# Kernel tuning notes

Measured on AMD Instinct MI355X. Metric: run time of the kernel, lower is better.

Reference implementation:

```python
import jax, jax.numpy as jnp
import numpy as np

B, N, D = 64, 197, 768
H, HD = 12, 64
MAX_REL = 14
SCALE = HD ** -0.5


def rel_indices(n, max_rel):
    """Static 2D relative-position index matrices of shape (n, n), int32."""
    lq = n - 1
    side = int(lq ** 0.5)
    r = np.arange(lq)
    dv = r[None, :] // side - r[:, None] // side
    dh = r[None, :] % side - r[:, None] % side
    fv = np.clip(dv, -max_rel, max_rel) + max_rel + 1
    fh = np.clip(dh, -max_rel, max_rel) + max_rel + 1
    # pad one row/col of zeros on top-left for the cls token (index 0)
    fv = np.pad(fv, ((1, 0), (1, 0)), constant_values=0)
    fh = np.pad(fh, ((1, 0), (1, 0)), constant_values=0)
    return fv.astype(np.int32), fh.astype(np.int32)


IDX_V, IDX_H = rel_indices(N, MAX_REL)


def setup_inputs() -> dict:
    key = jax.random.key(0)
    ks = jax.random.split(key, 13)
    lin = lambda k: jax.random.normal(k, (D, H * HD), jnp.float32) * 0.02
    tab = lambda k: jax.random.normal(k, (2 * MAX_REL + 2, HD), jnp.float32) * 0.02
    return {
        'x': jax.random.normal(ks[0], (B, N, D), jnp.float32),
        'wq': lin(ks[1]), 'bq': jnp.zeros((H * HD,), jnp.float32),
        'wk': lin(ks[2]), 'bk': jnp.zeros((H * HD,), jnp.float32),
        'wv': lin(ks[3]), 'bv': jnp.zeros((H * HD,), jnp.float32),
        'wp': jax.random.normal(ks[4], (H * HD, D), jnp.float32) * 0.02,
        'bp': jnp.zeros((D,), jnp.float32),
        'rel_k_v': tab(ks[5]), 'rel_k_h': tab(ks[6]),
        'rel_v_v': tab(ks[7]), 'rel_v_h': tab(ks[8]),
    }


def reference(x, wq, bq, wk, bk, wv, bv, wp, bp, rel_k_v, rel_k_h, rel_v_v, rel_v_h):
    b, n, _ = x.shape
    # qkv projections -> (B, H, N, HD)
    q = (x @ wq + bq).reshape(b, n, H, HD).transpose(0, 2, 1, 3)
    k = (x @ wk + bk).reshape(b, n, H, HD).transpose(0, 2, 1, 3)
    v = (x @ wv + bv).reshape(b, n, H, HD).transpose(0, 2, 1, 3)

    attn = jnp.einsum('bhid,bhjd->bhij', q, k) * SCALE
    # iRPE key bias: gather (N, N, HD) table then contract with q per query pos
    r_p_k = rel_k_v[IDX_V] + rel_k_h[IDX_H]              # (N, N, HD)
    attn = attn + jnp.einsum('bhid,ijd->bhij', q, r_p_k) * SCALE
    attn = jax.nn.softmax(attn, axis=-1)

    out = jnp.einsum('bhij,bhjd->bhid', attn, v)
    # iRPE value bias
    r_p_v = rel_v_v[IDX_V] + rel_v_h[IDX_H]              # (N, N, HD)
    out = out + jnp.einsum('bhij,ijd->bhid', attn, r_p_v)

    out = out.transpose(0, 2, 1, 3).reshape(b, n, H * HD)
    return out @ wp + bp
```

## Files before the change

kernel.cpp:

```cpp
#include <hip/hip_runtime.h>
#include <math.h>

#define SCALE_ 0.125f

typedef unsigned short u16;
typedef __attribute__((ext_vector_type(8))) _Float16 half8;
typedef __attribute__((ext_vector_type(4))) float f32x4;
#define MFMA_H __builtin_amdgcn_mfma_f32_16x16x32_f16

__device__ __forceinline__ u16 f2h(float f) {
    union { _Float16 h; u16 u; } v; v.h = (_Float16)f; return v.u;
}
__device__ __forceinline__ float h2f(u16 u) {
    union { _Float16 h; u16 u; } v; v.u = u; return (float)v.h;
}
__device__ __forceinline__ void gload16(const u16* g, u16* l) {
    __builtin_amdgcn_global_load_lds(
        (const __attribute__((address_space(1))) void*)g,
        (__attribute__((address_space(3))) void*)l, 16, 0, 0);
}
__device__ __forceinline__ half8 ld_h8(const u16* p) {
    return *(const half8*)p;
}

__global__ void prep_all(const float* __restrict__ x,
                         const float* __restrict__ w0, const float* __restrict__ w1,
                         const float* __restrict__ w2, const float* __restrict__ w3,
                         const float* __restrict__ rkv, const float* __restrict__ rkh,
                         const float* __restrict__ rvv, const float* __restrict__ rvh,
                         u16* __restrict__ xh,
                         u16* o0, u16* o1, u16* o2, u16* o3,
                         u16* __restrict__ tk, u16* __restrict__ gt,
                         u16* __restrict__ khot, u16* __restrict__ vtp) {
    __shared__ float t[64 * 68];
    int b = blockIdx.x;
    const int tid = threadIdx.x;

    if (b < 4728) {
        size_t idx = ((size_t)b * 256 + tid) * 8;
        float4 a = *(const float4*)(x + idx), bb = *(const float4*)(x + idx + 4);
        float f[8] = {a.x, a.y, a.z, a.w, bb.x, bb.y, bb.z, bb.w};
        u16 hs[8];
        #pragma unroll
        for (int e = 0; e < 8; ++e) hs[e] = f2h(f[e]);
        *(uint4*)(xh + idx) = *(uint4*)hs;
        return;
    }
    b -= 4728;
    if (b < 576) {
        int z = b / 144, rem = b - z * 144;
        int by = rem / 12, bx = rem - by * 12;
        const float* W; u16* oh;
        if (z == 0)      { W = w0; oh = o0; }
        else if (z == 1) { W = w1; oh = o1; }
        else if (z == 2) { W = w2; oh = o2; }
        else             { W = w3; oh = o3; }
        int k0 = by * 64, n0 = bx * 64;
        #pragma unroll
        for (int rr = 0; rr < 4; ++rr) {
            int r = (tid >> 4) + rr * 16;
            int c = (tid & 15) * 4;
            *(float4*)&t[r * 68 + c] = *(const float4*)(W + (size_t)(k0 + r) * 768 + n0 + c);
        }
        __syncthreads();
        int n = tid >> 2, kc = (tid & 3) * 16;
        u16 hs[16];
        #pragma unroll
        for (int e = 0; e < 16; ++e) hs[e] = f2h(t[(kc + e) * 68 + n]);
        size_t o = (size_t)(n0 + n) * 768 + k0 + kc;
        *(uint4*)(oh + o) = *(uint4*)hs;
        *(uint4*)(oh + o + 8) = *(uint4*)(hs + 8);
        return;
    }
    b -= 576;
    if (b < 16) {
        int idx = b * 256 + tid;
        int r = idx >> 6, d = idx & 63;
        float tv = 0.f;
        if (r < 30) tv = rkv[r * 64 + d];
        else if (r >= 32 && r < 62) tv = rkh[(r - 32) * 64 + d];
        tk[idx] = f2h(tv);
        return;
    }
    b -= 16;
    if (b < 28) {
        int idx = b * 256 + tid;
        int g = idx / 224, j = idx - (idx / 224) * 224;
        float v = 0.f;
        if (j >= 1 && j < 197) {
            int jq = j - 1;
            int jv = jq / 14, jh = jq - jv * 14;
            if (g < 14) v = (jv == g) ? 1.f : 0.f;
            else if (g >= 16 && g < 30) v = (jh == g - 16) ? 1.f : 0.f;
        }
        gt[idx] = f2h(v);
        return;
    }
    b -= 28;
    if (b < 28) {
        int idx = b * 256 + tid;
        int j = idx >> 5, c = idx & 31;
        float v = 0.f;
        if (j >= 1 && j < 197) {
            int jq = j - 1;
            int jv = jq / 14, jh = jq - jv * 14;
            if (c < 14) v = (jv == c) ? 1.f : 0.f;
            else if (c < 28) v = (jh == c - 14) ? 1.f : 0.f;
        }
        khot[idx] = f2h(v);
        return;
    }
    b -= 28;
    {
        u16* vb = vtp + (size_t)b * 64 * 288;
        for (int tt = tid; tt < 64 * 91; tt += 256) {
            int d = tt / 91;
            int c = 197 + (tt - d * 91);
            u16 val = 0;
            if (c >= 208 && c < 272) {
                int rr = c - 208;
                float v = 0.f;
                if (rr < 30) v = rvv[rr * 64 + d];
                else if (rr >= 32 && rr < 62) v = rvh[(rr - 32) * 64 + d];
                val = f2h(v);
            }
            vb[d * 288 + c] = val;
        }
    }
}

__global__ __launch_bounds__(256) void vtrans(const u16* __restrict__ v,
                                              u16* __restrict__ vt) {
    __shared__ u16 L[64 * 72];
    const int bh = blockIdx.x;
    const u16* src = v + (size_t)bh * 197 * 64;
    u16* dst = vt + (size_t)bh * 64 * 288;
    const int tid = threadIdx.x;
    const int keyl = tid >> 2;
    const int c8 = (tid & 3) * 16;
    for (int k0 = 0; k0 < 197; k0 += 64) {
        __syncthreads();
        int key = k0 + keyl;
        if (key < 197) {
            uint4 g0 = *(const uint4*)(src + key * 64 + c8);
            uint4 g1 = *(const uint4*)(src + key * 64 + c8 + 8);
            u16 t0[8]; *(uint4*)t0 = g0;
            u16 t1[8]; *(uint4*)t1 = g1;
            #pragma unroll
            for (int e = 0; e < 8; ++e) L[(c8 + e) * 72 + keyl] = t0[e];
            #pragma unroll
            for (int e = 0; e < 8; ++e) L[(c8 + 8 + e) * 72 + keyl] = t1[e];
        }
        __syncthreads();
        int d = tid >> 2, cc = (tid & 3) * 16;
        if (k0 + cc < 197) {
            int nvalid = min(16, 197 - k0 - cc);
            if (nvalid == 16) {
                *(uint4*)(dst + d * 288 + k0 + cc)     = *(const uint4*)&L[d * 72 + cc];
                *(uint4*)(dst + d * 288 + k0 + cc + 8) = *(const uint4*)&L[d * 72 + cc + 8];
            } else {
                for (int e = 0; e < nvalid; ++e)
                    dst[d * 288 + k0 + cc + e] = L[d * 72 + cc + e];
            }
        }
    }
}

__global__ __launch_bounds__(256, 4) void gemm_f16(
    const u16* __restrict__ Ah,
    const u16* __restrict__ B0, const u16* __restrict__ B1, const u16* __restrict__ B2,
    const float* __restrict__ bias0, const float* __restrict__ bias1,
    const float* __restrict__ bias2,
    u16* qo, u16* ko, u16* vo, float* outf, int nz, int kind)
{
    __shared__ u16 SM[128 * 64 * 2];
    u16* As = SM;
    u16* Bs = SM + 128 * 64;

    const int p = blockIdx.x;
    const int xcd = p & 7, s = p >> 3;
    const int mcnt = (xcd < 3) ? 13 : 12;
    const int mbase = (xcd < 3) ? xcd * 13 : 39 + (xcd - 3) * 12;
    const int jn = 6 * nz;
    if (s >= mcnt * jn) return;
    const int mb = mbase + s / jn;
    const int j = s % jn;
    const int z = j / 6;
    const int nb = j % 6;

    const u16* Bt = B0; const float* bias = bias0;
    if (z == 1) { Bt = B1; bias = bias1; }
    else if (z == 2) { Bt = B2; bias = bias2; }

    const int m0 = mb * 128, n0 = nb * 128;
    const int tid = threadIdx.x;
    const int w = tid >> 6, lane = tid & 63, quad = lane >> 4, l16 = lane & 15;
    const int wm = (w >> 1) * 64, wn = (w & 1) * 64;
    const int rl8 = lane >> 3, cs = lane & 7;
    const int csrc = (cs ^ rl8) * 8;

    f32x4 acc[4][4];
    #pragma unroll
    for (int a = 0; a < 4; ++a)
        #pragma unroll
        for (int b = 0; b < 4; ++b) acc[a][b] = (f32x4){0, 0, 0, 0};

    for (int kt = 0; kt < 768; kt += 64) {
        __syncthreads();
        #pragma unroll
        for (int i = 0; i < 4; ++i) {
            int r = w * 32 + i * 8 + rl8;
            int arow = min(m0 + r, 12607);
            gload16(Ah + (size_t)arow * 768 + kt + csrc, &As[(w * 32 + i * 8) * 64]);
            gload16(Bt + (size_t)(n0 + r) * 768 + kt + csrc, &Bs[(w * 32 + i * 8) * 64]);
        }
        __syncthreads();
        #pragma unroll
        for (int kb = 0; kb < 2; ++kb) {
            const int slot = ((kb * 4 + quad) ^ (l16 & 7)) * 8;
            half8 ah[4], bf[4];
            #pragma unroll
            for (int mi = 0; mi < 4; ++mi) {
                ah[mi] = ld_h8(&As[(wm + mi * 16 + l16) * 64 + slot]);
                bf[mi] = ld_h8(&Bs[(wn + mi * 16 + l16) * 64 + slot]);
            }
            #pragma unroll
            for (int ni = 0; ni < 4; ++ni)
                #pragma unroll
                for (int mi = 0; mi < 4; ++mi)
                    acc[mi][ni] = MFMA_H(ah[mi], bf[ni], acc[mi][ni], 0, 0, 0);
        }
    }

    if (kind == 1) {
        #pragma unroll
        for (int mi = 0; mi < 4; ++mi) {
            #pragma unroll
            for (int r = 0; r < 4; ++r) {
                int gr = m0 + wm + mi * 16 + quad * 4 + r;
                if (gr >= 12608) continue;
                #pragma unroll
                for (int ni = 0; ni < 4; ++ni) {
                    int gc = n0 + wn + ni * 16 + l16;
                    outf[(size_t)gr * 768 + gc] = acc[mi][ni][r] + bias[gc];
                }
            }
        }
        return;
    }

    __syncthreads();
    u16* Cs = SM;
    #pragma unroll
    for (int mi = 0; mi < 4; ++mi) {
        #pragma unroll
        for (int ni = 0; ni < 4; ++ni) {
            int col = wn + ni * 16 + l16;
            float bv = bias[n0 + col];
            #pragma unroll
            for (int r = 0; r < 4; ++r)
                Cs[(wm + mi * 16 + quad * 4 + r) * 128 + col] = f2h(acc[mi][ni][r] + bv);
        }
    }
    __syncthreads();
    u16* O = (z == 0) ? qo : ((z == 1) ? ko : vo);
    int row = tid >> 1, halfc = tid & 1;
    int gr = m0 + row;
    if (gr < 12608) {
        int bb = gr / 197, ii = gr - bb * 197;
        int h = (n0 >> 6) + halfc;
        u16* dst = O + ((size_t)(bb * 12 + h) * 197 + ii) * 64;
        const u16* src = &Cs[row * 128 + halfc * 64];
        #pragma unroll
        for (int e = 0; e < 8; ++e)
            *(uint4*)(dst + e * 8) = *(const uint4*)(src + e * 8);
    }
}

__global__ __launch_bounds__(512, 3) void attn_mfma(
    const u16* __restrict__ qh, const u16* __restrict__ kh,
    const u16* __restrict__ tk, const u16* __restrict__ vt,
    const u16* __restrict__ gt, const u16* __restrict__ khot,
    u16* __restrict__ oh)
{
    __shared__ u16 Ph[64 * 296];
    __shared__ float BsT[64 * 36];
    __shared__ float red[64 * 4];
    u16* Tvh16 = (u16*)BsT;
    u16* Kst = Ph;

    const int p = blockIdx.x;
    const int xcd = p & 7, s = p >> 3;
    const int bh = xcd * 96 + (s >> 2);
    const int qt = s & 3;
    const int I0 = qt * 64;
    const int tid = threadIdx.x;
    const int w = tid >> 6, lane = tid & 63, quad = lane >> 4, l16 = lane & 15;
    const int mf = w >> 1, nh = w & 1;
    const int mr0 = mf * 16;
    const size_t base = (size_t)bh * 197 * 64;
    const uint4 z4 = make_uint4(0, 0, 0, 0);

    half8 qa[2];
    {
        int i = I0 + mr0 + l16;
        bool ok = i < 197;
        const u16* qp = qh + base + (size_t)i * 64 + quad * 8;
        #pragma unroll
        for (int kb = 0; kb < 2; ++kb) {
            uint4 a = ok ? *(const uint4*)(qp + kb * 32) : z4;
            *(uint4*)&qa[kb] = a;
        }
    }
    int jj[7];
    #pragma unroll
    for (int s1 = 0; s1 < 7; ++s1) jj[s1] = (nh * 7 + s1) * 16 + l16;
    half8 kfh[7];
    #pragma unroll
    for (int s1 = 0; s1 < 7; ++s1)
        kfh[s1] = ld_h8(khot + jj[s1] * 32 + quad * 8);
    uint4 kreg[4];
    #pragma unroll
    for (int t2 = 0; t2 < 4; ++t2) {
        int t = tid + t2 * 512;
        int row = t >> 3, chunk = t & 7;
        kreg[t2] = (t < 1792 && row < 197)
                 ? *(const uint4*)(kh + base + (size_t)row * 64 + chunk * 8) : z4;
    }

    #pragma unroll
    for (int s2 = 0; s2 < 2; ++s2) {
        int c = (nh * 2 + s2) * 16 + l16;
        f32x4 acc = (f32x4){0, 0, 0, 0};
        #pragma unroll
        for (int kb = 0; kb < 2; ++kb) {
            half8 th = ld_h8(tk + c * 64 + kb * 32 + quad * 8);
            acc = MFMA_H(qa[kb], th, acc, 0, 0, 0);
        }
        #pragma unroll
        for (int r = 0; r < 4; ++r)
            Tvh16[(mr0 + quad * 4 + r) * 68 + c] = f2h(acc[r]);
    }

    #pragma unroll
    for (int t2 = 0; t2 < 4; ++t2) {
        int t = tid + t2 * 512;
        if (t < 1792) {
            int row = t >> 3, chunk = t & 7;
            *(uint4*)&Kst[row * 72 + chunk * 8] = kreg[t2];
        }
    }
    __syncthreads();

    half8 qa2;
    {
        int m = mr0 + l16;
        int i = I0 + m;
        u16 vals[8];
        if (i >= 1 && i < 197) {
            int qi = i - 1;
            int iv = qi / 14, ih = qi - iv * 14;
            #pragma unroll
            for (int e = 0; e < 8; ++e) {
                int c = quad * 8 + e;
                u16 v = 0;
                if (c < 14)      v = Tvh16[m * 68 + (c - iv + 15)];
                else if (c < 28) v = Tvh16[m * 68 + 32 + ((c - 14) - ih + 15)];
                vals[e] = v;
            }
        } else {
            #pragma unroll
            for (int e = 0; e < 8; ++e) vals[e] = 0;
        }
        *(uint4*)&qa2 = *(uint4*)vals;
    }

    f32x4 sacc[7];
    #pragma unroll
    for (int s1 = 0; s1 < 7; ++s1) {
        int j = jj[s1];
        f32x4 c = MFMA_H(qa[0], ld_h8(&Kst[j * 72 + quad * 8]),
                         (f32x4){0, 0, 0, 0}, 0, 0, 0);
        c = MFMA_H(qa[1], ld_h8(&Kst[j * 72 + 32 + quad * 8]), c, 0, 0, 0);
        c = MFMA_H(qa2, kfh[s1], c, 0, 0, 0);
        sacc[s1] = c;
    }

    #pragma unroll
    for (int r = 0; r < 4; ++r) {
        float mx = sacc[0][r];
        #pragma unroll
        for (int s1 = 1; s1 < 7; ++s1) mx = fmaxf(mx, sacc[s1][r]);
        mx *= SCALE_;
        #pragma unroll
        for (int off = 1; off < 16; off <<= 1) mx = fmaxf(mx, __shfl_xor(mx, off, 64));
        if (l16 == 0) red[(mr0 + quad * 4 + r) * 4 + nh] = mx;
    }
    __syncthreads();

    #pragma unroll
    for (int r = 0; r < 4; ++r) {
        int m = mr0 + quad * 4 + r;
        float M = fmaxf(red[m * 4], red[m * 4 + 1]);
        float sum = 0.f;
        #pragma unroll
        for (int s1 = 0; s1 < 7; ++s1) {
            float pv = (jj[s1] < 197) ? __expf(sacc[s1][r] * SCALE_ - M) : 0.f;
            sacc[s1][r] = pv;
            sum += pv;
        }
        #pragma unroll
        for (int off = 1; off < 16; off <<= 1) sum += __shfl_xor(sum, off, 64);
        if (l16 == 0) red[m * 4 + 2 + nh] = sum;
    }
    #pragma unroll
    for (int s1 = 0; s1 < 7; ++s1) {
        int j = jj[s1];
        if (j < 208) {
            #pragma unroll
            for (int r = 0; r < 4; ++r)
                Ph[(mr0 + quad * 4 + r) * 296 + j] = f2h(sacc[s1][r]);
        }
    }
    #pragma unroll
    for (int t = 0; t < 2; ++t) {
        int ii2 = tid + t * 512;
        Ph[(ii2 >> 4) * 296 + 208 + (ii2 & 15)] = 0;
    }
    __syncthreads();

    {
        f32x4 bacc = (f32x4){0, 0, 0, 0};
        #pragma unroll
        for (int ks = 0; ks < 7; ++ks) {
            half8 ap = ld_h8(&Ph[(mr0 + l16) * 296 + ks * 32 + quad * 8]);
            half8 gp = ld_h8(gt + (nh * 16 + l16) * 224 + ks * 32 + quad * 8);
            bacc = MFMA_H(ap, gp, bacc, 0, 0, 0);
        }
        #pragma unroll
        for (int r = 0; r < 4; ++r)
            BsT[(mr0 + quad * 4 + r) * 36 + nh * 16 + l16] = bacc[r];
    }
    for (int t = tid; t < 64 * 16; t += 512)
        Ph[(t >> 4) * 296 + 272 + (t & 15)] = 0;
    __syncthreads();

    #pragma unroll
    for (int t = 0; t < 8; ++t) {
        int idx = tid + t * 512;
        int m = idx >> 6, c = idx & 63;
        int i = I0 + m;
        float val;
        if (i == 0) {
            val = (c == 0 || c == 32) ? (red[m * 4 + 2] + red[m * 4 + 3]) : 0.f;
        } else {
            int qi = i - 1;
            int iv = qi / 14, ih = qi - (qi / 14) * 14;
            int r = c & 31;
            int bidx = r + ((c < 32) ? iv : ih) - 15;
            bool ok = (bidx >= 0) && (bidx <= 13) && (r < 30);
            int src = ((c < 32) ? 0 : 16) + min(13, max(0, bidx));
            val = ok ? BsT[m * 36 + src] : 0.f;
            if (r == 0) val += h2f(Ph[m * 296]);
        }
        Ph[m * 296 + 208 + c] = f2h(val);
    }
    __syncthreads();

    {
        f32x4 oacc[2] = {(f32x4){0, 0, 0, 0}, (f32x4){0, 0, 0, 0}};
        const u16* vb = vt + (size_t)bh * 64 * 288;
        #pragma unroll
        for (int ks = 0; ks < 9; ++ks) {
            half8 ap = ld_h8(&Ph[(mr0 + l16) * 296 + ks * 32 + quad * 8]);
            #pragma unroll
            for (int sd = 0; sd < 2; ++sd) {
                int d = (nh * 2 + sd) * 16 + l16;
                half8 bv = ld_h8(vb + (size_t)d * 288 + ks * 32 + quad * 8);
                oacc[sd] = MFMA_H(ap, bv, oacc[sd], 0, 0, 0);
            }
        }
        int b = bh / 12, h = bh - b * 12;
        float rl[4];
        #pragma unroll
        for (int r = 0; r < 4; ++r) {
            int m = mr0 + quad * 4 + r;
            rl[r] = 1.f / (red[m * 4 + 2] + red[m * 4 + 3]);
        }
        #pragma unroll
        for (int sd = 0; sd < 2; ++sd) {
            int d = (nh * 2 + sd) * 16 + l16;
            #pragma unroll
            for (int r = 0; r < 4; ++r) {
                int i = I0 + mr0 + quad * 4 + r;
                if (i < 197) {
                    oh[((size_t)(b * 197 + i)) * 768 + h * 64 + d] =
                        f2h(oacc[sd][r] * rl[r]);
                }
            }
        }
    }
}

extern "C" void kernel_launch(void* const* d_in, const int* in_sizes, int n_in,
                              void* d_out, int out_size, void* d_ws, size_t ws_size,
                              hipStream_t stream)
{
    const float* x   = (const float*)d_in[0];
    const float* wq  = (const float*)d_in[1];
    const float* bq  = (const float*)d_in[2];
    const float* wk  = (const float*)d_in[3];
    const float* bk  = (const float*)d_in[4];
    const float* wv  = (const float*)d_in[5];
    const float* bv  = (const float*)d_in[6];
    const float* wp  = (const float*)d_in[7];
    const float* bp  = (const float*)d_in[8];
    const float* rkv = (const float*)d_in[9];
    const float* rkh = (const float*)d_in[10];
    const float* rvv = (const float*)d_in[11];
    const float* rvh = (const float*)d_in[12];
    float* out = (float*)d_out;

    const size_t SZX = (size_t)12608 * 768;
    const size_t SZW = (size_t)768 * 768;
    const size_t SZVT = (size_t)768 * 64 * 288;

    u16* xh  = (u16*)d_ws;
    u16* qh_ = xh + SZX;
    u16* kh_ = qh_ + SZX;
    u16* vh_ = kh_ + SZX;
    u16* vt  = vh_ + SZX;
    u16* wt  = vt + SZVT;
    u16* wqh = wt;
    u16* wkh = wt + SZW;
    u16* wvh = wt + 2 * SZW;
    u16* wph = wt + 3 * SZW;
    u16* tk  = wt + 4 * SZW;
    u16* gt  = tk + 4096;
    u16* khot = gt + 32 * 224;
    u16* oh_ = xh;

    prep_all<<<6144, 256, 0, stream>>>(
        x, wq, wk, wv, wp, rkv, rkh, rvv, rvh,
        xh, wqh, wkh, wvh, wph, tk, gt, khot, vt);

    gemm_f16<<<1872, 256, 0, stream>>>(
        xh, wqh, wkh, wvh, bq, bk, bv, qh_, kh_, vh_, nullptr, 3, 0);

    vtrans<<<768, 256, 0, stream>>>(vh_, vt);

    attn_mfma<<<3072, 512, 0, stream>>>(qh_, kh_, tk, vt, gt, khot, oh_);

    gemm_f16<<<624, 256, 0, stream>>>(
        oh_, wph, wph, wph, bp, bp, bp, nullptr, nullptr, nullptr, out, 1, 1);
}
```

Before: 293.7 us.

## Fuse V transpose into QKV GEMM epilogue and async-load swizzled K tile

```diff
diff --git a/kernel.cpp b/kernel.cpp
--- a/kernel.cpp
+++ b/kernel.cpp
@@ -129,43 +129,6 @@
     }
 }
 
-__global__ __launch_bounds__(256) void vtrans(const u16* __restrict__ v,
-                                              u16* __restrict__ vt) {
-    __shared__ u16 L[64 * 72];
-    const int bh = blockIdx.x;
-    const u16* src = v + (size_t)bh * 197 * 64;
-    u16* dst = vt + (size_t)bh * 64 * 288;
-    const int tid = threadIdx.x;
-    const int keyl = tid >> 2;
-    const int c8 = (tid & 3) * 16;
-    for (int k0 = 0; k0 < 197; k0 += 64) {
-        __syncthreads();
-        int key = k0 + keyl;
-        if (key < 197) {
-            uint4 g0 = *(const uint4*)(src + key * 64 + c8);
-            uint4 g1 = *(const uint4*)(src + key * 64 + c8 + 8);
-            u16 t0[8]; *(uint4*)t0 = g0;
-            u16 t1[8]; *(uint4*)t1 = g1;
-            #pragma unroll
-            for (int e = 0; e < 8; ++e) L[(c8 + e) * 72 + keyl] = t0[e];
-            #pragma unroll
-            for (int e = 0; e < 8; ++e) L[(c8 + 8 + e) * 72 + keyl] = t1[e];
-        }
-        __syncthreads();
-        int d = tid >> 2, cc = (tid & 3) * 16;
-        if (k0 + cc < 197) {
-            int nvalid = min(16, 197 - k0 - cc);
-            if (nvalid == 16) {
-                *(uint4*)(dst + d * 288 + k0 + cc)     = *(const uint4*)&L[d * 72 + cc];
-                *(uint4*)(dst + d * 288 + k0 + cc + 8) = *(const uint4*)&L[d * 72 + cc + 8];
-            } else {
-                for (int e = 0; e < nvalid; ++e)
-                    dst[d * 288 + k0 + cc + e] = L[d * 72 + cc + e];
-            }
-        }
-    }
-}
-
 __global__ __launch_bounds__(256, 4) void gemm_f16(
     const u16* __restrict__ Ah,
     const u16* __restrict__ B0, const u16* __restrict__ B1, const u16* __restrict__ B2,
@@ -263,7 +226,24 @@
         }
     }
     __syncthreads();
-    u16* O = (z == 0) ? qo : ((z == 1) ? ko : vo);
+
+    if (z == 2) {
+        int k2 = tid & 127, chalf = tid >> 7;
+        int gr = m0 + k2;
+        if (gr < 12608) {
+            int bb = gr / 197, ii = gr - bb * 197;
+            int h = (n0 >> 6) + chalf;
+            u16* vbase = vo + ((size_t)(bb * 12 + h) * 64) * 288 + ii;
+            #pragma unroll
+            for (int dd = 0; dd < 64; ++dd) {
+                int d = (dd + (k2 & 63)) & 63;
+                vbase[(size_t)d * 288] = Cs[k2 * 128 + chalf * 64 + d];
+            }
+        }
+        return;
+    }
+
+    u16* O = (z == 0) ? qo : ko;
     int row = tid >> 1, halfc = tid & 1;
     int gr = m0 + row;
     if (gr < 12608) {
@@ -319,14 +299,17 @@
     #pragma unroll
     for (int s1 = 0; s1 < 7; ++s1)
         kfh[s1] = ld_h8(khot + jj[s1] * 32 + quad * 8);
-    uint4 kreg[4];
+
     #pragma unroll
     for (int t2 = 0; t2 < 4; ++t2) {
         int t = tid + t2 * 512;
         int row = t >> 3, chunk = t & 7;
-        kreg[t2] = (t < 1792 && row < 197)
-                 ? *(const uint4*)(kh + base + (size_t)row * 64 + chunk * 8) : z4;
-    }
+        if (t < 1792 && row < 197)
+            gload16(kh + base + (size_t)row * 64 + ((chunk ^ (row & 7)) * 8),
+                    &Kst[(w * 64 + t2 * 512) * 8]);
+    }
+    if (tid < 216)
+        *(uint4*)&Kst[197 * 64 + tid * 8] = z4;
 
     #pragma unroll
     for (int s2 = 0; s2 < 2; ++s2) {
@@ -340,15 +323,6 @@
         #pragma unroll
         for (int r = 0; r < 4; ++r)
             Tvh16[(mr0 + quad * 4 + r) * 68 + c] = f2h(acc[r]);
-    }
-
-    #pragma unroll
-    for (int t2 = 0; t2 < 4; ++t2) {
-        int t = tid + t2 * 512;
-        if (t < 1792) {
-            int row = t >> 3, chunk = t & 7;
-            *(uint4*)&Kst[row * 72 + chunk * 8] = kreg[t2];
-        }
     }
     __syncthreads();
 
@@ -379,9 +353,9 @@
     #pragma unroll
     for (int s1 = 0; s1 < 7; ++s1) {
         int j = jj[s1];
-        f32x4 c = MFMA_H(qa[0], ld_h8(&Kst[j * 72 + quad * 8]),
+        f32x4 c = MFMA_H(qa[0], ld_h8(&Kst[j * 64 + ((quad ^ (j & 7)) * 8)]),
                          (f32x4){0, 0, 0, 0}, 0, 0, 0);
-        c = MFMA_H(qa[1], ld_h8(&Kst[j * 72 + 32 + quad * 8]), c, 0, 0, 0);
+        c = MFMA_H(qa[1], ld_h8(&Kst[j * 64 + (((quad + 4) ^ (j & 7)) * 8)]), c, 0, 0, 0);
         c = MFMA_H(qa2, kfh[s1], c, 0, 0, 0);
         sacc[s1] = c;
     }
@@ -528,8 +502,7 @@
     u16* xh  = (u16*)d_ws;
     u16* qh_ = xh + SZX;
     u16* kh_ = qh_ + SZX;
-    u16* vh_ = kh_ + SZX;
-    u16* vt  = vh_ + SZX;
+    u16* vt  = kh_ + SZX;
     u16* wt  = vt + SZVT;
     u16* wqh = wt;
     u16* wkh = wt + SZW;
@@ -545,9 +518,7 @@
         xh, wqh, wkh, wvh, wph, tk, gt, khot, vt);
 
     gemm_f16<<<1872, 256, 0, stream>>>(
-        xh, wqh, wkh, wvh, bq, bk, bv, qh_, kh_, vh_, nullptr, 3, 0);
-
-    vtrans<<<768, 256, 0, stream>>>(vh_, vt);
+        xh, wqh, wkh, wvh, bq, bk, bv, qh_, kh_, vt, nullptr, 3, 0);
 
     attn_mfma<<<3072, 512, 0, stream>>>(qh_, kh_, tk, vt, gt, khot, oh_);
 
```

New measurement: 349.9 us. 1.19x slower.
